# Optimization experiments

Hardware: AMD Instinct MI355X
Metric: run time of the kernel (lower is better)

The kernel has to match this reference:

```python
import jax, jax.numpy as jnp
import numpy as np

B, S, D_MODEL = 2, 2048, 2048
N_HEADS, N_KV = 16, 4
HEAD_DIM = D_MODEL // N_HEADS  # 128
N_REP = N_HEADS // N_KV        # 4


def _apply_rope(x, cos, sin):
    # x: [B, H, S, Dh]; cos/sin: [S, Dh//2]
    c = cos[None, None, :, :]
    s = sin[None, None, :, :]
    x_even = x[..., ::2]
    x_odd = x[..., 1::2]
    re = x_even * c - x_odd * s
    ro = x_even * s + x_odd * c
    # interleave back: stack on last axis then flatten -> [..., Dh]
    return jnp.stack([re, ro], axis=-1).reshape(x.shape)


def setup_inputs() -> dict:
    key = jax.random.key(0)
    ks = jax.random.split(key, 7)
    std = 1.0 / np.sqrt(D_MODEL)
    return {
        "x": jax.random.normal(ks[0], (B, S, D_MODEL), dtype=jnp.float32),
        "rope_cos": jax.random.uniform(ks[1], (S, HEAD_DIM // 2), dtype=jnp.float32),
        "rope_sin": jax.random.uniform(ks[2], (S, HEAD_DIM // 2), dtype=jnp.float32),
        "Wq": jax.random.normal(ks[3], (D_MODEL, N_HEADS * HEAD_DIM), dtype=jnp.float32) * std,
        "Wk": jax.random.normal(ks[4], (D_MODEL, N_KV * HEAD_DIM), dtype=jnp.float32) * std,
        "Wv": jax.random.normal(ks[5], (D_MODEL, N_KV * HEAD_DIM), dtype=jnp.float32) * std,
        "Wo": jax.random.normal(ks[6], (N_HEADS * HEAD_DIM, D_MODEL), dtype=jnp.float32) * std,
    }


def reference(x, rope_cos, rope_sin, Wq, Wk, Wv, Wo):
    batch, seq_len, _ = x.shape
    q = (x @ Wq).reshape(batch, seq_len, N_HEADS, HEAD_DIM).transpose(0, 2, 1, 3)
    k = (x @ Wk).reshape(batch, seq_len, N_KV, HEAD_DIM).transpose(0, 2, 1, 3)
    v = (x @ Wv).reshape(batch, seq_len, N_KV, HEAD_DIM).transpose(0, 2, 1, 3)

    q = _apply_rope(q, rope_cos[:seq_len], rope_sin[:seq_len])
    k = _apply_rope(k, rope_cos[:seq_len], rope_sin[:seq_len])

    # GQA: group q heads by kv head instead of materializing repeated k/v.
    qg = q.reshape(batch, N_KV, N_REP, seq_len, HEAD_DIM)
    scale = 1.0 / np.sqrt(HEAD_DIM)
    scores = jnp.einsum('bgrqd,bgkd->bgrqk', qg, k) * scale

    causal = jnp.tril(jnp.ones((seq_len, seq_len), dtype=bool))
    scores = jnp.where(causal[None, None, None, :, :], scores, -jnp.inf)
    weights = jax.nn.softmax(scores, axis=-1)

    out = jnp.einsum('bgrqk,bgkd->bgrqd', weights, v)
    out = out.reshape(batch, N_HEADS, seq_len, HEAD_DIM).transpose(0, 2, 1, 3)
    out = out.reshape(batch, seq_len, N_HEADS * HEAD_DIM)
    return out @ Wo
```

## Files before the change

kernel.cpp:

```cpp
#include <hip/hip_runtime.h>
#include <hip/hip_bf16.h>
#include <math.h>

typedef __bf16 bf16x8_t __attribute__((ext_vector_type(8)));
typedef float f32x4 __attribute__((ext_vector_type(4)));
typedef unsigned short ushort8 __attribute__((ext_vector_type(8)));

__device__ inline unsigned short f2bf(float f) {
  unsigned int u = __builtin_bit_cast(unsigned int, f);
  u += 0x7fffu + ((u >> 16) & 1u);
  return (unsigned short)(u >> 16);
}
__device__ inline float b2f(unsigned short s) {
  unsigned int u = ((unsigned int)s) << 16;
  return __builtin_bit_cast(float, u);
}
__device__ inline unsigned int pack2bf(float lo, float hi) {
  return (unsigned int)f2bf(lo) | ((unsigned int)f2bf(hi) << 16);
}

__device__ __forceinline__ void gll16(const void* g, void* l) {
  __builtin_amdgcn_global_load_lds((const __attribute__((address_space(1))) void*)g,
                                   (__attribute__((address_space(3))) void*)l, 16, 0, 0);
}

__global__ void cvt_k(const float* __restrict__ X, unsigned short* __restrict__ Xb, int total8) {
  int i = blockIdx.x * blockDim.x + threadIdx.x;
  if (i >= total8) return;
  const float4* p = (const float4*)X + 2 * (size_t)i;
  float4 a = p[0], b = p[1];
  ushort8 v;
  v[0] = f2bf(a.x); v[1] = f2bf(a.y); v[2] = f2bf(a.z); v[3] = f2bf(a.w);
  v[4] = f2bf(b.x); v[5] = f2bf(b.y); v[6] = f2bf(b.z); v[7] = f2bf(b.w);
  ((ushort8*)Xb)[i] = v;
}

__global__ void twc_k(const float* __restrict__ W, unsigned short* __restrict__ Wt, int K, int N) {
  __shared__ float tile[32][33];
  int k0 = blockIdx.x * 32, n0 = blockIdx.y * 32;
  int tx = threadIdx.x, ty = threadIdx.y;
#pragma unroll
  for (int i = 0; i < 32; i += 8) tile[ty + i][tx] = W[(size_t)(k0 + ty + i) * N + n0 + tx];
  __syncthreads();
#pragma unroll
  for (int i = 0; i < 32; i += 8)
    Wt[(size_t)(n0 + ty + i) * K + k0 + tx] = f2bf(tile[tx][ty + i]);
}

template <bool OUT_BF16, bool ROPE>
__global__ __launch_bounds__(256) void gemm_tn(const unsigned short* __restrict__ A,
                                               const unsigned short* __restrict__ Bt,
                                               void* __restrict__ Cv, int M, int N, int K,
                                               const float* __restrict__ cs,
                                               const float* __restrict__ sn, int ropeLim) {
  __shared__ __align__(16) unsigned short As[2][128 * 32];
  __shared__ __align__(16) unsigned short Bs[2][128 * 32];
  const int t = threadIdx.x, w = t >> 6, lane = t & 63;
  const int la = lane & 15, lk = lane >> 4;
  const int wr = w >> 1, wc = w & 1;
  const int bm = blockIdx.y * 128, bn = blockIdx.x * 128;
  const int lrow = lane >> 2, lcb = (lane & 3) * 8;

  const unsigned short* Ab = A + (size_t)(bm + (w * 2) * 16 + lrow) * K + lcb;
  const unsigned short* Ab1 = A + (size_t)(bm + (w * 2 + 1) * 16 + lrow) * K + lcb;
  const unsigned short* Bb = Bt + (size_t)(bn + (w * 2) * 16 + lrow) * K + lcb;
  const unsigned short* Bb1 = Bt + (size_t)(bn + (w * 2 + 1) * 16 + lrow) * K + lcb;
  const int c0 = w * 2, c1 = w * 2 + 1;

  f32x4 acc[4][4] = {};

  gll16(Ab, (char*)As[0] + c0 * 1024);
  gll16(Ab1, (char*)As[0] + c1 * 1024);
  gll16(Bb, (char*)Bs[0] + c0 * 1024);
  gll16(Bb1, (char*)Bs[0] + c1 * 1024);

  const int nt = K / 32;
  int cur = 0;
  for (int kt = 0; kt < nt; ++kt) {
    __syncthreads();
    if (kt + 1 < nt) {
      const int kn = (kt + 1) * 32;
      gll16(Ab + kn, (char*)As[cur ^ 1] + c0 * 1024);
      gll16(Ab1 + kn, (char*)As[cur ^ 1] + c1 * 1024);
      gll16(Bb + kn, (char*)Bs[cur ^ 1] + c0 * 1024);
      gll16(Bb1 + kn, (char*)Bs[cur ^ 1] + c1 * 1024);
    }

    bf16x8_t a[4], b[4];
#pragma unroll
    for (int m = 0; m < 4; ++m)
      a[m] = __builtin_bit_cast(
          bf16x8_t, *(const ushort8*)(As[cur] + (wr * 64 + m * 16 + la) * 32 + lk * 8));
#pragma unroll
    for (int n = 0; n < 4; ++n)
      b[n] = __builtin_bit_cast(
          bf16x8_t, *(const ushort8*)(Bs[cur] + (wc * 64 + n * 16 + la) * 32 + lk * 8));
#pragma unroll
    for (int m = 0; m < 4; ++m)
#pragma unroll
      for (int n = 0; n < 4; ++n)
        acc[m][n] = __builtin_amdgcn_mfma_f32_16x16x32_bf16(a[m], b[n], acc[m][n], 0, 0, 0);
    cur ^= 1;
  }

#pragma unroll
  for (int m = 0; m < 4; ++m) {
#pragma unroll
    for (int n = 0; n < 4; ++n) {
      const int col = bn + wc * 64 + n * 16 + la;
      const bool doRope = ROPE && (col < ropeLim);
#pragma unroll
      for (int r = 0; r < 4; ++r) {
        int row = bm + wr * 64 + m * 16 + lk * 4 + r;
        float val = acc[m][n][r];
        if (ROPE) {
          float pval = __shfl_xor(val, 1);
          if (doRope) {
            int srow = row & 2047;
            int i = (col & 127) >> 1;
            float cc = cs[srow * 64 + i], ss = sn[srow * 64 + i];
            val = (la & 1) ? (pval * ss + val * cc) : (val * cc - pval * ss);
          }
        }
        if (OUT_BF16)
          ((unsigned short*)Cv)[(size_t)row * N + col] = f2bf(val);
        else
          ((float*)Cv)[(size_t)row * N + col] = val;
      }
    }
  }
}

__global__ void transpose_v(const unsigned short* __restrict__ QKV, unsigned short* __restrict__ Vt) {
  __shared__ unsigned short tile[32][33];
  int bg = blockIdx.z;
  int b = bg >> 2, g = bg & 3;
  int s0 = blockIdx.x * 32, d0 = blockIdx.y * 32;
  int tx = threadIdx.x, ty = threadIdx.y;
#pragma unroll
  for (int i = 0; i < 32; i += 8)
    tile[ty + i][tx] = QKV[((size_t)(b * 2048 + s0 + ty + i)) * 3072 + 2560 + g * 128 + d0 + tx];
  __syncthreads();
#pragma unroll
  for (int i = 0; i < 32; i += 8)
    Vt[((size_t)(bg * 128 + d0 + ty + i)) * 2048 + s0 + tx] = tile[tx][ty + i];
}

__global__ __launch_bounds__(256, 2) void attn_mfma(const unsigned short* __restrict__ QKV,
                                                    const unsigned short* __restrict__ Vt,
                                                    unsigned short* __restrict__ Ob,
                                                    unsigned short* __restrict__ oP,
                                                    float* __restrict__ mlP) {
  const int S = 2048;
  __shared__ __align__(16) unsigned short Ks[2][64 * 128];
  __shared__ __align__(16) unsigned short Vs[2][128 * 64];
  __shared__ __align__(16) unsigned short Ps[4 * 32 * 64];

  const int t = threadIdx.x;
  const int w = t >> 6, lane = t & 63;
  const int la = lane & 15, lk = lane >> 4;
  const int b = blockIdx.z, h = blockIdx.y, g = h >> 2;

  int x = blockIdx.x, qt, c;
  if (x < 9) { qt = 7 + x; c = 0; }
  else if (x == 9) { qt = 15; c = 1; }
  else { int k = (x - 10) >> 1; if ((x & 1) == 0) { qt = 6 - k; c = 0; } else { qt = 14 - k; c = 1; } }

  const int qw = qt * 128 + w * 32;
  const int n_full = 2 * qt + 2;
  const int kts = c * 16;
  const int kte = min(n_full, kts + 16);
  const bool full = (kts == 0) && (kte == n_full);
  const float scale = 0.08838834764831845f;

  const unsigned short* ksrc[4];
  const unsigned short* vsrc[4];
#pragma unroll
  for (int u = 0; u < 4; ++u) {
    int kr = 16 * w + 4 * u + (lane >> 4);
    int kp = lane & 15;
    ksrc[u] = QKV + (size_t)(b * S + kr) * 3072 + 2048 + g * 128 + (kp ^ (kr & 7)) * 8;
    int vr = 32 * w + 8 * u + (lane >> 3);
    int vp = lane & 7;
    vsrc[u] = Vt + (size_t)((b * 4 + g) * 128 + vr) * 2048 + (vp ^ (vr & 7)) * 8;
  }

  bf16x8_t qf[2][4];
#pragma unroll
  for (int qi = 0; qi < 2; ++qi)
#pragma unroll
    for (int dt = 0; dt < 4; ++dt)
      qf[qi][dt] = __builtin_bit_cast(
          bf16x8_t, *(const ushort8*)(QKV + (size_t)(b * S + qw + qi * 16 + la) * 3072 + h * 128 +
                                      dt * 32 + lk * 8));

  f32x4 oa[2][8];
#pragma unroll
  for (int qi = 0; qi < 2; ++qi)
#pragma unroll
    for (int dt = 0; dt < 8; ++dt) oa[qi][dt] = (f32x4){0.f, 0.f, 0.f, 0.f};
  float mr[2] = {-1e30f, -1e30f}, lr[2] = {0.f, 0.f};

  const int kmask0 = qw & ~63;
  char* pw = (char*)Ps + w * 4096;

#pragma unroll
  for (int u = 0; u < 4; ++u) {
    gll16(ksrc[u] + (size_t)(kts * 64) * 3072, (char*)Ks[0] + (4 * w + u) * 1024);
    gll16(vsrc[u] + kts * 64, (char*)Vs[0] + (4 * w + u) * 1024);
  }
  __syncthreads();

  int cur = 0;
  for (int kt = kts; kt < kte; ++kt) {
    const int k0 = kt * 64;
    if (kt + 1 < kte) {
      const int kn = k0 + 64;
#pragma unroll
      for (int u = 0; u < 4; ++u) {
        gll16(ksrc[u] + (size_t)kn * 3072, (char*)Ks[cur ^ 1] + (4 * w + u) * 1024);
        gll16(vsrc[u] + kn, (char*)Vs[cur ^ 1] + (4 * w + u) * 1024);
      }
    }

    if (k0 <= qw + 31) {
      char* Ksb = (char*)Ks[cur];
      char* Vsb = (char*)Vs[cur];

      f32x4 sacc[2][4];
#pragma unroll
      for (int qi = 0; qi < 2; ++qi)
#pragma unroll
        for (int ktc = 0; ktc < 4; ++ktc) sacc[qi][ktc] = (f32x4){0.f, 0.f, 0.f, 0.f};
      __builtin_amdgcn_s_setprio(1);
#pragma unroll
      for (int ktc = 0; ktc < 4; ++ktc) {
        int row = ktc * 16 + la;
#pragma unroll
        for (int dt = 0; dt < 4; ++dt) {
          bf16x8_t kf = __builtin_bit_cast(
              bf16x8_t, *(const ushort8*)(Ksb + row * 256 + ((((dt << 2) + lk) ^ (row & 7)) << 4)));
          sacc[0][ktc] = __builtin_amdgcn_mfma_f32_16x16x32_bf16(kf, qf[0][dt], sacc[0][ktc], 0, 0, 0);
          sacc[1][ktc] = __builtin_amdgcn_mfma_f32_16x16x32_bf16(kf, qf[1][dt], sacc[1][ktc], 0, 0, 0);
        }
      }
      __builtin_amdgcn_s_setprio(0);

      const bool domask = (k0 == kmask0);
#pragma unroll
      for (int qi = 0; qi < 2; ++qi) {
        const int q = qw + qi * 16 + la;
        float p[4][4];
        float tm = -1e30f;
#pragma unroll
        for (int ktc = 0; ktc < 4; ++ktc)
#pragma unroll
          for (int r = 0; r < 4; ++r) {
            float sv = sacc[qi][ktc][r] * scale;
            if (domask && (k0 + ktc * 16 + lk * 4 + r > q)) sv = -1e30f;
            p[ktc][r] = sv;
            tm = fmaxf(tm, sv);
          }
        tm = fmaxf(tm, __shfl_xor(tm, 16));
        tm = fmaxf(tm, __shfl_xor(tm, 32));
        float mn;
        if (__all(tm - mr[qi] <= 8.f)) {
          mn = mr[qi];
        } else {
          mn = fmaxf(mr[qi], tm);
          float sc = __expf(mr[qi] - mn);
          mr[qi] = mn;
          lr[qi] *= sc;
          float scb[4];
#pragma unroll
          for (int r = 0; r < 4; ++r) scb[r] = __shfl(sc, lk * 4 + r);
#pragma unroll
          for (int dt = 0; dt < 8; ++dt)
#pragma unroll
            for (int r = 0; r < 4; ++r) oa[qi][dt][r] *= scb[r];
        }
        float ts = 0.f;
#pragma unroll
        for (int ktc = 0; ktc < 4; ++ktc)
#pragma unroll
          for (int r = 0; r < 4; ++r) {
            float e = __expf(p[ktc][r] - mn);
            p[ktc][r] = e;
            ts += e;
          }
        ts += __shfl_xor(ts, 16);
        ts += __shfl_xor(ts, 32);
        lr[qi] += ts;
        char* pq = pw + (qi * 16 + la) * 128;
#pragma unroll
        for (int ktc = 0; ktc < 4; ++ktc) {
          uint2 gv;
          gv.x = pack2bf(p[ktc][0], p[ktc][1]);
          gv.y = pack2bf(p[ktc][2], p[ktc][3]);
          *(uint2*)(pq + ((32 * ktc + 8 * lk) ^ ((la & 7) << 4))) = gv;
        }
      }
      asm volatile("s_waitcnt lgkmcnt(0)" ::: "memory");

      bf16x8_t pf[2][2];
#pragma unroll
      for (int qi = 0; qi < 2; ++qi)
#pragma unroll
        for (int ks = 0; ks < 2; ++ks)
          pf[qi][ks] = __builtin_bit_cast(
              bf16x8_t, *(const ushort8*)(pw + (qi * 16 + la) * 128 +
                                          ((64 * ks + 16 * lk) ^ ((la & 7) << 4))));
      __builtin_amdgcn_s_setprio(1);
#pragma unroll
      for (int dt = 0; dt < 8; ++dt) {
        int d = dt * 16 + la;
#pragma unroll
        for (int ks = 0; ks < 2; ++ks) {
          bf16x8_t vf = __builtin_bit_cast(
              bf16x8_t, *(const ushort8*)(Vsb + d * 128 + ((((ks << 2) + lk) ^ (d & 7)) << 4)));
          oa[0][dt] = __builtin_amdgcn_mfma_f32_16x16x32_bf16(pf[0][ks], vf, oa[0][dt], 0, 0, 0);
          oa[1][dt] = __builtin_amdgcn_mfma_f32_16x16x32_bf16(pf[1][ks], vf, oa[1][dt], 0, 0, 0);
        }
      }
      __builtin_amdgcn_s_setprio(0);
    }

    __syncthreads();
    cur ^= 1;
  }

  if (full) {
#pragma unroll
    for (int qi = 0; qi < 2; ++qi) {
      float inv = 1.f / lr[qi];
      float invb[4];
#pragma unroll
      for (int r = 0; r < 4; ++r) invb[r] = __shfl(inv, lk * 4 + r);
#pragma unroll
      for (int dt = 0; dt < 8; ++dt)
#pragma unroll
        for (int r = 0; r < 4; ++r)
          Ob[(size_t)(b * S + qw + qi * 16 + lk * 4 + r) * 2048 + h * 128 + dt * 16 + la] =
              f2bf(oa[qi][dt][r] * invb[r]);
    }
  } else {
    const int slot = (b * 16 + h) * 8 + (qt - 8);
    unsigned short* op = oP + ((size_t)slot * 2 + c) * (128 * 128);
    float* ml = mlP + ((size_t)slot * 2 + c) * 256;
#pragma unroll
    for (int qi = 0; qi < 2; ++qi) {
      if (lk == 0) {
        ml[w * 32 + qi * 16 + la] = mr[qi];
        ml[128 + w * 32 + qi * 16 + la] = lr[qi];
      }
      float inv = 1.f / lr[qi];
      float invb[4];
#pragma unroll
      for (int r = 0; r < 4; ++r) invb[r] = __shfl(inv, lk * 4 + r);
#pragma unroll
      for (int dt = 0; dt < 8; ++dt)
#pragma unroll
        for (int r = 0; r < 4; ++r)
          op[(size_t)(w * 32 + qi * 16 + lk * 4 + r) * 128 + dt * 16 + la] =
              f2bf(oa[qi][dt][r] * invb[r]);
    }
  }
}

__global__ __launch_bounds__(256) void combine_k(const unsigned short* __restrict__ oP,
                                                 const float* __restrict__ mlP,
                                                 unsigned short* __restrict__ Ob) {
  const int slot = blockIdx.x;
  const int b = slot >> 7, h = (slot >> 3) & 15, qt = 8 + (slot & 7);
  const int t = threadIdx.x;
  const int r = t >> 1, half = t & 1;
  const float* ml0 = mlP + (size_t)slot * 512;
  const float* ml1 = ml0 + 256;
  float m0 = ml0[r], l0 = ml0[128 + r], m1 = ml1[r], l1 = ml1[128 + r];
  float M = fmaxf(m0, m1);
  float w0 = l0 * __expf(m0 - M), w1 = l1 * __expf(m1 - M);
  float inv = 1.f / (w0 + w1);
  w0 *= inv;
  w1 *= inv;
  const unsigned short* o0 = oP + (size_t)slot * 2 * 16384 + r * 128 + half * 64;
  const unsigned short* o1 = o0 + 16384;
  unsigned short* ob = Ob + (size_t)(b * 2048 + qt * 128 + r) * 2048 + h * 128 + half * 64;
#pragma unroll
  for (int j = 0; j < 64; j += 8) {
    ushort8 a = *(const ushort8*)(o0 + j);
    ushort8 c = *(const ushort8*)(o1 + j);
    ushort8 o;
#pragma unroll
    for (int e = 0; e < 8; ++e) o[e] = f2bf(w0 * b2f(a[e]) + w1 * b2f(c[e]));
    *(ushort8*)(ob + j) = o;
  }
}

extern "C" void kernel_launch(void* const* d_in, const int* in_sizes, int n_in,
                              void* d_out, int out_size, void* d_ws, size_t ws_size,
                              hipStream_t stream) {
  const float* x = (const float*)d_in[0];
  const float* rc = (const float*)d_in[1];
  const float* rs = (const float*)d_in[2];
  const float* Wq = (const float*)d_in[3];
  const float* Wk = (const float*)d_in[4];
  const float* Wv = (const float*)d_in[5];
  const float* Wo = (const float*)d_in[6];
  float* out = (float*)d_out;

  const int B = 2, S = 2048, DM = 2048;
  const int M = B * S;

  unsigned short* xb = (unsigned short*)d_ws;
  unsigned short* QKV = xb + (size_t)M * DM;
  unsigned short* WallT = QKV + (size_t)M * 3072;
  unsigned short* WoT = WallT;
  unsigned short* Vt = WallT + (size_t)2048 * 2048;
  unsigned short* Ob = xb;
  unsigned short* oP = WallT + (size_t)3072 * 2048;
  float* mlP = (float*)(oP + (size_t)256 * 2 * 16384);

  dim3 blk(256);

  cvt_k<<<(M * DM / 8 + 255) / 256, blk, 0, stream>>>(x, xb, M * DM / 8);
  twc_k<<<dim3(64, 64), dim3(32, 8), 0, stream>>>(Wq, WallT, DM, DM);
  twc_k<<<dim3(64, 16), dim3(32, 8), 0, stream>>>(Wk, WallT + (size_t)2048 * DM, DM, 512);
  twc_k<<<dim3(64, 16), dim3(32, 8), 0, stream>>>(Wv, WallT + (size_t)2560 * DM, DM, 512);

  gemm_tn<true, true><<<dim3(3072 / 128, M / 128), blk, 0, stream>>>(xb, WallT, QKV, M, 3072, DM,
                                                                     rc, rs, 2560);

  twc_k<<<dim3(64, 64), dim3(32, 8), 0, stream>>>(Wo, WoT, DM, DM);

  transpose_v<<<dim3(S / 32, 4, B * 4), dim3(32, 8), 0, stream>>>(QKV, Vt);

  attn_mfma<<<dim3(24, 16, B), blk, 0, stream>>>(QKV, Vt, Ob, oP, mlP);
  combine_k<<<dim3(256), blk, 0, stream>>>(oP, mlP, Ob);

  gemm_tn<false, false><<<dim3(DM / 128, M / 128), blk, 0, stream>>>(Ob, WoT, out, M, DM, DM,
                                                                     nullptr, nullptr, 0);
}
```

Before: 265.9 us.

## Single-buffer K/V tiles in LDS with split staging between QK and PV phases

Measured after the change: 261.3 us. Within noise of the previous version (-1.7%).

```diff
diff --git a/kernel.cpp b/kernel.cpp
--- a/kernel.cpp
+++ b/kernel.cpp
@@ -152,8 +152,8 @@
                                                     unsigned short* __restrict__ oP,
                                                     float* __restrict__ mlP) {
   const int S = 2048;
-  __shared__ __align__(16) unsigned short Ks[2][64 * 128];
-  __shared__ __align__(16) unsigned short Vs[2][128 * 64];
+  __shared__ __align__(16) unsigned short Ks[64 * 128];
+  __shared__ __align__(16) unsigned short Vs[128 * 64];
   __shared__ __align__(16) unsigned short Ps[4 * 32 * 64];
 
   const int t = threadIdx.x;
@@ -185,6 +185,19 @@
     vsrc[u] = Vt + (size_t)((b * 4 + g) * 128 + vr) * 2048 + (vp ^ (vr & 7)) * 8;
   }
 
+#define STAGE_K(KT)                                                              \
+  do {                                                                           \
+    const size_t _o = (size_t)(KT) * 64 * 3072;                                  \
+    _Pragma("unroll") for (int u = 0; u < 4; ++u)                                \
+        gll16(ksrc[u] + _o, (char*)Ks + (4 * w + u) * 1024);                     \
+  } while (0)
+#define STAGE_V(KT)                                                              \
+  do {                                                                           \
+    const size_t _o = (size_t)(KT) * 64;                                         \
+    _Pragma("unroll") for (int u = 0; u < 4; ++u)                                \
+        gll16(vsrc[u] + _o, (char*)Vs + (4 * w + u) * 1024);                     \
+  } while (0)
+
   bf16x8_t qf[2][4];
 #pragma unroll
   for (int qi = 0; qi < 2; ++qi)
@@ -203,30 +216,19 @@
 
   const int kmask0 = qw & ~63;
   char* pw = (char*)Ps + w * 4096;
-
-#pragma unroll
-  for (int u = 0; u < 4; ++u) {
-    gll16(ksrc[u] + (size_t)(kts * 64) * 3072, (char*)Ks[0] + (4 * w + u) * 1024);
-    gll16(vsrc[u] + kts * 64, (char*)Vs[0] + (4 * w + u) * 1024);
-  }
+  char* Ksb = (char*)Ks;
+  char* Vsb = (char*)Vs;
+
+  STAGE_K(kts);
+  STAGE_V(kts);
   __syncthreads();
 
-  int cur = 0;
   for (int kt = kts; kt < kte; ++kt) {
     const int k0 = kt * 64;
-    if (kt + 1 < kte) {
-      const int kn = k0 + 64;
-#pragma unroll
-      for (int u = 0; u < 4; ++u) {
-        gll16(ksrc[u] + (size_t)kn * 3072, (char*)Ks[cur ^ 1] + (4 * w + u) * 1024);
-        gll16(vsrc[u] + kn, (char*)Vs[cur ^ 1] + (4 * w + u) * 1024);
-      }
-    }
-
-    if (k0 <= qw + 31) {
-      char* Ksb = (char*)Ks[cur];
-      char* Vsb = (char*)Vs[cur];
-
+    const bool active = (k0 <= qw + 31);
+
+    bf16x8_t pf[2][2];
+    if (active) {
       f32x4 sacc[2][4];
 #pragma unroll
       for (int qi = 0; qi < 2; ++qi)
@@ -301,8 +303,6 @@
         }
       }
       asm volatile("s_waitcnt lgkmcnt(0)" ::: "memory");
-
-      bf16x8_t pf[2][2];
 #pragma unroll
       for (int qi = 0; qi < 2; ++qi)
 #pragma unroll
@@ -310,6 +310,12 @@
           pf[qi][ks] = __builtin_bit_cast(
               bf16x8_t, *(const ushort8*)(pw + (qi * 16 + la) * 128 +
                                           ((64 * ks + 16 * lk) ^ ((la & 7) << 4))));
+    }
+
+    __syncthreads();
+    if (kt + 1 < kte) STAGE_K(kt + 1);
+
+    if (active) {
       __builtin_amdgcn_s_setprio(1);
 #pragma unroll
       for (int dt = 0; dt < 8; ++dt) {
@@ -326,7 +332,7 @@
     }
 
     __syncthreads();
-    cur ^= 1;
+    if (kt + 1 < kte) STAGE_V(kt + 1);
   }
 
   if (full) {
@@ -365,6 +371,8 @@
               f2bf(oa[qi][dt][r] * invb[r]);
     }
   }
+#undef STAGE_K
+#undef STAGE_V
 }
 
 __global__ __launch_bounds__(256) void combine_k(const unsigned short* __restrict__ oP,
```
